# Optimization experiments

Hardware: AMD Instinct MI355X
Metric: run time of the kernel (lower is better)

The kernel has to match this reference:

```python
import jax, jax.numpy as jnp
import numpy as np

N = 50000          # nodes
M_UND = 500000     # undirected edges -> E = 2*M_UND directed messages
Q = 16             # num_groups
MAX_ITER = 10
BP_MAX_DIFF = 0.01


def setup_inputs() -> dict:
    key = jax.random.key(0)
    k1, k2, k3, k4 = jax.random.split(key, 4)
    u = jax.random.randint(k1, (M_UND,), 0, N)
    v = jax.random.randint(k2, (M_UND,), 0, N)
    # each undirected edge (u,v) yields directed messages u->v and v->u
    src = jnp.concatenate([u, v]).astype(jnp.int32)
    dst = jnp.concatenate([v, u]).astype(jnp.int32)
    rev = jnp.concatenate([jnp.arange(M_UND) + M_UND, jnp.arange(M_UND)]).astype(jnp.int32)
    psi0 = jax.random.uniform(k3, (N, Q), dtype=jnp.float32)
    psi0 = psi0 / psi0.sum(1, keepdims=True)
    msg0 = jax.random.uniform(k4, (2 * M_UND, Q), dtype=jnp.float32)
    msg0 = msg0 / msg0.sum(1, keepdims=True)
    c = 2.0 * M_UND / N  # mean degree
    beta = jnp.float32(np.log(Q / np.sqrt(c - 1.0) + 1.0))  # beta_ast init
    return dict(src=src, dst=dst, rev=rev, psi0=psi0, msg0=msg0, beta=beta, n_nodes=N)


def _bp_forward(src, dst, rev, psi0, msg0, beta, n_nodes):
    q = psi0.shape[1]
    n_edges = msg0.shape[0]
    mean_w = float(n_edges) / (float(n_nodes) * float(n_nodes))  # W.mean() for 0/1 weights
    expb_m1 = jnp.exp(beta) - 1.0
    h0 = (-beta * mean_w * psi0).sum(0)  # external field, shape [q]

    def step(carry, _):
        msg, psi, h, done = carry
        # S_e = 1 + psi_{src->dst} * (e^{beta*w} - 1), w == 1
        logS = jnp.log1p(msg * expb_m1)                                    # [E, q]
        node_log = jax.ops.segment_sum(logS, dst, num_segments=n_nodes)    # prod over incoming, log-domain
        # cavity update: message i->j uses all incoming to i except j->i (rev edge)
        new_msg = jax.nn.softmax(node_log[src] - logS[rev] + h, axis=-1)   # exp(h)*prod, normalized
        diff = jnp.max(jnp.abs(jax.lax.stop_gradient(new_msg) -
                               jax.lax.stop_gradient(msg)).sum(-1))
        logS2 = jnp.log1p(new_msg * expb_m1)
        node_log2 = jax.ops.segment_sum(logS2, dst, num_segments=n_nodes)
        new_psi = jax.nn.softmax(node_log2 + h, axis=-1)                    # marginals
        new_h = (-beta * mean_w * new_psi).sum(0)
        # freeze state once converged (mirrors early-return on max_diff < bp_max_diff)
        msg = jnp.where(done, msg, new_msg)
        psi = jnp.where(done, psi, new_psi)
        h = jnp.where(done, h, new_h)
        done = done | (diff < BP_MAX_DIFF)
        return (msg, psi, h, done), diff

    (msg, psi, h, done), _ = jax.lax.scan(
        step, (msg0, psi0, h0, jnp.array(False)), None, length=MAX_ITER)

    # soft modularity: (1/2m) sum_e psi_i . psi_j - sum_g (sum_i d_i psi_ig / 2m)^2
    m2 = float(n_edges)  # total directed edge weight (= 2m for unit weights)
    deg = jax.ops.segment_sum(jnp.ones((n_edges,), psi.dtype), dst, num_segments=n_nodes)
    edge_term = jnp.einsum('eq,eq->', psi[src], psi[dst]) / m2
    deg_term = jnp.sum((jnp.einsum('n,nq->q', deg, psi) / m2) ** 2)
    modularity = edge_term - deg_term
    # group-balance regularizer, scaled by sqrt(q) as in forward()
    reg = jnp.sum((psi.sum(0) / float(n_nodes) - 1.0 / q) ** 2) * np.sqrt(q)
    # mean per-node entropy of marginals, normalized by log(q)
    entropy_loss = jnp.mean(-jnp.sum(psi * jnp.log(psi + 1e-12), axis=-1)) / np.log(q)
    return psi, reg, entropy_loss, modularity


def reference(src, dst, rev, psi0, msg0, beta, n_nodes):
    return _bp_forward(src, dst, rev, psi0, msg0, beta, n_nodes)
```

## Files before the change

kernel.cpp:

```cpp
#include <hip/hip_runtime.h>

#define Q 16
#define SCAN_B 256

__device__ __forceinline__ float wsum(float v){
  #pragma unroll
  for(int o=32;o;o>>=1) v += __shfl_xor(v,o);
  return v;
}
__device__ __forceinline__ float wmaxr(float v){
  #pragma unroll
  for(int o=32;o;o>>=1) v = fmaxf(v,__shfl_xor(v,o));
  return v;
}

__global__ void __launch_bounds__(256, 8) k_edgeF(
    const int* __restrict__ src, const int* __restrict__ dst,
    const int* __restrict__ ipos,
    float* msgC, const float* __restrict__ nl,
    const float* __restrict__ betap,
    const float* __restrict__ hsrc, int nch,
    const float* __restrict__ diffprev, int nbd,
    float* __restrict__ diffout, float* __restrict__ hout,
    int* __restrict__ donep, int M, float mean_w, int k)
{
  if (*donep) return;
  const float beta = *betap;
  const float eb = __expf(beta) - 1.0f;
  const int t = threadIdx.x;
  __shared__ float smf[16][17];
  __shared__ float hq_sm[16];
  __shared__ float smx[4];
  __shared__ int brk;
  {
    const int g = t>>4, qq = t&15;
    float s = 0.0f;
    for (int r = g; r < nch; r += 16) s += hsrc[(size_t)r*Q + qq];
    smf[g][qq] = s; __syncthreads();
    if (t < Q){
      float tot = 0.0f;
      #pragma unroll
      for (int i=0;i<16;i++) tot += smf[i][t];
      hq_sm[t] = -beta * mean_w * tot;
    }
  }
  if (k > 0){
    float dm = 0.0f;
    for (int i = t; i < nbd; i += 256) dm = fmaxf(dm, diffprev[i]);
    dm = wmaxr(dm);
    if ((t & 63) == 0) smx[t>>6] = dm;
    __syncthreads();
    if (t == 0)
      brk = (fmaxf(fmaxf(smx[0],smx[1]), fmaxf(smx[2],smx[3])) < 0.01f);
    __syncthreads();
    if (brk){ if (blockIdx.x == 0 && t == 0) *donep = 1; return; }
  } else {
    __syncthreads();
  }
  if (blockIdx.x == 0 && t < Q) hout[t] = hq_sm[t];
  const float hq = hq_sm[t & 15];

  const int q = t & 15;
  const int grp  = (blockIdx.x*blockDim.x + t) >> 4;
  const int ngrp = (gridDim.x*blockDim.x) >> 4;
  float dloc = 0.0f;
  int p = grp;
  for (; p + ngrp < M; p += 2*ngrp){
    const int pA = p, pB = p + ngrp;
    const int uA = src[pA], vA = dst[pA];
    const int uB = src[pB], vB = dst[pB];
    const int a0 = ipos[pA], a1 = ipos[pA + M];
    const int b0 = ipos[pB], b1 = ipos[pB + M];
    const float mA0 = msgC[(size_t)a0*Q + q], mA1 = msgC[(size_t)a1*Q + q];
    const float mB0 = msgC[(size_t)b0*Q + q], mB1 = msgC[(size_t)b1*Q + q];
    const float nuA = nl[(size_t)uA*Q + q],  nvA = nl[(size_t)vA*Q + q];
    const float nuB = nl[(size_t)uB*Q + q],  nvB = nl[(size_t)vB*Q + q];
    float tA0 = nuA - __logf(fmaf(mA1, eb, 1.0f)) + hq;
    float tA1 = nvA - __logf(fmaf(mA0, eb, 1.0f)) + hq;
    float tB0 = nuB - __logf(fmaf(mB1, eb, 1.0f)) + hq;
    float tB1 = nvB - __logf(fmaf(mB0, eb, 1.0f)) + hq;
    float xA0=tA0, xA1=tA1, xB0=tB0, xB1=tB1;
    #pragma unroll
    for (int o=1;o<16;o<<=1){
      xA0=fmaxf(xA0,__shfl_xor(xA0,o)); xA1=fmaxf(xA1,__shfl_xor(xA1,o));
      xB0=fmaxf(xB0,__shfl_xor(xB0,o)); xB1=fmaxf(xB1,__shfl_xor(xB1,o));
    }
    const float eA0=__expf(tA0-xA0), eA1=__expf(tA1-xA1);
    const float eB0=__expf(tB0-xB0), eB1=__expf(tB1-xB1);
    float sA0=eA0, sA1=eA1, sB0=eB0, sB1=eB1;
    #pragma unroll
    for (int o=1;o<16;o<<=1){
      sA0+=__shfl_xor(sA0,o); sA1+=__shfl_xor(sA1,o);
      sB0+=__shfl_xor(sB0,o); sB1+=__shfl_xor(sB1,o);
    }
    const float nA0=eA0/sA0, nA1=eA1/sA1, nB0=eB0/sB0, nB1=eB1/sB1;
    float dA0=fabsf(nA0-mA0), dA1=fabsf(nA1-mA1);
    float dB0=fabsf(nB0-mB0), dB1=fabsf(nB1-mB1);
    #pragma unroll
    for (int o=1;o<16;o<<=1){
      dA0+=__shfl_xor(dA0,o); dA1+=__shfl_xor(dA1,o);
      dB0+=__shfl_xor(dB0,o); dB1+=__shfl_xor(dB1,o);
    }
    dloc = fmaxf(dloc, fmaxf(fmaxf(dA0,dA1), fmaxf(dB0,dB1)));
    msgC[(size_t)a0*Q + q] = nA0;  msgC[(size_t)a1*Q + q] = nA1;
    msgC[(size_t)b0*Q + q] = nB0;  msgC[(size_t)b1*Q + q] = nB1;
  }
  if (p < M){
    const int u = src[p], v = dst[p];
    const int i0 = ipos[p], i1 = ipos[p + M];
    const float m0 = msgC[(size_t)i0*Q + q], m1 = msgC[(size_t)i1*Q + q];
    const float nu = nl[(size_t)u*Q + q],   nv = nl[(size_t)v*Q + q];
    float t0 = nu - __logf(fmaf(m1, eb, 1.0f)) + hq;
    float t1 = nv - __logf(fmaf(m0, eb, 1.0f)) + hq;
    float x0=t0, x1=t1;
    #pragma unroll
    for (int o=1;o<16;o<<=1){
      x0=fmaxf(x0,__shfl_xor(x0,o)); x1=fmaxf(x1,__shfl_xor(x1,o));
    }
    const float e0=__expf(t0-x0), e1=__expf(t1-x1);
    float s0=e0, s1=e1;
    #pragma unroll
    for (int o=1;o<16;o<<=1){ s0+=__shfl_xor(s0,o); s1+=__shfl_xor(s1,o); }
    const float n0=e0/s0, n1=e1/s1;
    float d0=fabsf(n0-m0), d1=fabsf(n1-m1);
    #pragma unroll
    for (int o=1;o<16;o<<=1){ d0+=__shfl_xor(d0,o); d1+=__shfl_xor(d1,o); }
    dloc = fmaxf(dloc, fmaxf(d0,d1));
    msgC[(size_t)i0*Q + q] = n0;  msgC[(size_t)i1*Q + q] = n1;
  }
  float wm = wmaxr(dloc);
  if ((t & 63) == 0) smx[t>>6] = wm;
  __syncthreads();
  if (t == 0)
    diffout[blockIdx.x] = fmaxf(fmaxf(smx[0],smx[1]), fmaxf(smx[2],smx[3]));
}

__global__ void __launch_bounds__(256, 8) k_gatherF2(
    const float* __restrict__ msgC, const int* __restrict__ offs,
    float* __restrict__ nl, const float* __restrict__ hk,
    float* __restrict__ psi, const float* __restrict__ betap,
    const int* __restrict__ donep, float* __restrict__ hp2k,
    int N, int mode)
{
  if (mode && *donep) return;
  const int wid = threadIdx.x >> 6;
  const int n = blockIdx.x*4 + wid;
  const float eb = __expf(*betap) - 1.0f;
  const int lane = threadIdx.x & 63;
  const int sub = lane >> 4, q16 = lane & 15;
  int start = 0, end = 0;
  if (n < N){ start = offs[n]; end = offs[n+1]; }
  float acc = 0.0f;
  int i = start + sub;
  for (; i + 4 < end; i += 8){
    const float x0 = msgC[(size_t)i*Q + q16];
    const float x1 = msgC[(size_t)(i+4)*Q + q16];
    acc += __logf(fmaf(x0, eb, 1.0f)) + __logf(fmaf(x1, eb, 1.0f));
  }
  if (i < end) acc += __logf(fmaf(msgC[(size_t)i*Q + q16], eb, 1.0f));
  acc += __shfl_xor(acc, 16);
  acc += __shfl_xor(acc, 32);
  if (n < N && sub == 0) nl[(size_t)n*Q + q16] = acc;
  if (!mode) return;
  float t = acc + hk[q16];
  float m = t;
  #pragma unroll
  for (int o=1;o<16;o<<=1) m = fmaxf(m, __shfl_xor(m,o));
  float ex = __expf(t-m);
  float s = ex;
  #pragma unroll
  for (int o=1;o<16;o<<=1) s += __shfl_xor(s,o);
  const float pq = ex/s;
  if (n < N && sub == 0) psi[(size_t)n*Q + q16] = pq;
  __shared__ float smh[4][17];
  if (sub == 0) smh[wid][q16] = (n < N) ? pq : 0.0f;
  __syncthreads();
  if (threadIdx.x < Q)
    unsafeAtomicAdd(&hp2k[(size_t)(blockIdx.x>>6)*Q + threadIdx.x],
      smh[0][threadIdx.x]+smh[1][threadIdx.x]+smh[2][threadIdx.x]+smh[3][threadIdx.x]);
}

__global__ void __launch_bounds__(256, 8) k_h_part(
    const float* __restrict__ psi, float* __restrict__ hpart, int N)
{
  const int n = blockIdx.x*blockDim.x + threadIdx.x;
  float pv[Q];
  if (n < N) {
    const float4* a = (const float4*)(psi + (size_t)n*Q);
    #pragma unroll
    for (int i=0;i<4;i++){ float4 t=a[i]; pv[4*i]=t.x; pv[4*i+1]=t.y; pv[4*i+2]=t.z; pv[4*i+3]=t.w; }
  } else {
    #pragma unroll
    for (int q=0;q<Q;q++) pv[q]=0.0f;
  }
  __shared__ float sm[4][Q];
  const int wid = threadIdx.x>>6, lane = threadIdx.x&63;
  #pragma unroll
  for (int q=0;q<Q;q++){
    float s = wsum(pv[q]);
    if (lane == 0) sm[wid][q] = s;
  }
  __syncthreads();
  if (threadIdx.x < Q)
    hpart[(size_t)blockIdx.x*Q + threadIdx.x] =
      sm[0][threadIdx.x]+sm[1][threadIdx.x]+sm[2][threadIdx.x]+sm[3][threadIdx.x];
}

__global__ void __launch_bounds__(256, 8) k_deg(
    const int* __restrict__ dst, int* __restrict__ deg, int E)
{
  const int e = blockIdx.x*blockDim.x + threadIdx.x;
  if (e < E) atomicAdd(&deg[dst[e]], 1);
}

__global__ void __launch_bounds__(SCAN_B) k_scan1(
    const int* __restrict__ deg, int* __restrict__ offs,
    int* __restrict__ bsum, int N)
{
  __shared__ int sm[SCAN_B];
  const int i = blockIdx.x*SCAN_B + threadIdx.x;
  const int v = (i<N) ? deg[i] : 0;
  sm[threadIdx.x] = v; __syncthreads();
  #pragma unroll
  for (int o=1;o<SCAN_B;o<<=1){
    int t = (threadIdx.x>=o) ? sm[threadIdx.x-o] : 0;
    __syncthreads();
    sm[threadIdx.x] += t;
    __syncthreads();
  }
  if (i<N) offs[i] = sm[threadIdx.x] - v;
  if (threadIdx.x==SCAN_B-1) bsum[blockIdx.x] = sm[threadIdx.x];
}

__global__ void __launch_bounds__(SCAN_B) k_scan2(int* __restrict__ bsum, int nb)
{
  __shared__ int sm[SCAN_B];
  const int v = (threadIdx.x<nb) ? bsum[threadIdx.x] : 0;
  sm[threadIdx.x] = v; __syncthreads();
  #pragma unroll
  for (int o=1;o<SCAN_B;o<<=1){
    int t = (threadIdx.x>=o) ? sm[threadIdx.x-o] : 0;
    __syncthreads();
    sm[threadIdx.x] += t;
    __syncthreads();
  }
  if (threadIdx.x<nb) bsum[threadIdx.x] = sm[threadIdx.x] - v;
}

__global__ void __launch_bounds__(SCAN_B) k_scan3(
    int* __restrict__ offs, int* __restrict__ cursor,
    const int* __restrict__ bsum, int N, int E)
{
  const int i = blockIdx.x*SCAN_B + threadIdx.x;
  if (i<N){
    const int o = offs[i] + bsum[blockIdx.x];
    offs[i] = o; cursor[i] = o;
  }
  if (i==0) offs[N] = E;
}

__global__ void __launch_bounds__(256, 8) k_fillCS(
    const int* __restrict__ dst, int* __restrict__ cursor,
    const float* __restrict__ msg0, float* __restrict__ msgC,
    int* __restrict__ ipos, int E)
{
  const int e = blockIdx.x*blockDim.x + threadIdx.x;
  if (e >= E) return;
  const int ip = atomicAdd(&cursor[dst[e]], 1);
  ipos[e] = ip;
  const float4* s = (const float4*)(msg0 + (size_t)e*Q);
  float4* d = (float4*)(msgC + (size_t)ip*Q);
  float4 x0=s[0], x1=s[1], x2=s[2], x3=s[3];
  d[0]=x0; d[1]=x1; d[2]=x2; d[3]=x3;
}

__global__ void __launch_bounds__(256, 8) k_stats(
    const int* __restrict__ src, const int* __restrict__ dst,
    const float* __restrict__ psi, const int* __restrict__ deg,
    float* __restrict__ colpart, float* __restrict__ degpart,
    float* __restrict__ entpart, float* __restrict__ edgepart,
    int* __restrict__ cnt, float* __restrict__ out,
    int M, int N, int NQ, float m2, int gS)
{
  const int t = threadIdx.x;
  const int lane = t & 63, wid = t >> 6;
  float ed = 0.0f;
  for (int p = blockIdx.x*256 + t; p < M; p += gS*256){
    const int u = src[p], v = dst[p];
    const float4* a = (const float4*)(psi + (size_t)u*Q);
    const float4* b = (const float4*)(psi + (size_t)v*Q);
    float d = 0.0f;
    #pragma unroll
    for (int i=0;i<4;i++){
      float4 x=a[i], y=b[i];
      d += x.x*y.x + x.y*y.y + x.z*y.z + x.w*y.w;
    }
    ed += 2.0f*d;
  }
  float ca[Q], da[Q]; float ea = 0.0f;
  #pragma unroll
  for (int q=0;q<Q;q++){ ca[q]=0.0f; da[q]=0.0f; }
  for (int n = blockIdx.x*256 + t; n < N; n += gS*256){
    const float4* a = (const float4*)(psi + (size_t)n*Q);
    float pv[Q];
    #pragma unroll
    for (int i=0;i<4;i++){ float4 x=a[i]; pv[4*i]=x.x; pv[4*i+1]=x.y; pv[4*i+2]=x.z; pv[4*i+3]=x.w; }
    const float dg = (float)deg[n];
    #pragma unroll
    for (int q=0;q<Q;q++){
      ca[q] += pv[q];
      da[q] += pv[q]*dg;
      ea    -= pv[q]*__logf(pv[q]+1e-12f);
    }
  }
  __shared__ float smc[4][17], smd[4][17];
  __shared__ float sme[4], smeE[4];
  __shared__ float smg[16][17], smg2[16][17];
  __shared__ int amL;
  #pragma unroll
  for (int q=0;q<Q;q++){
    float s  = wsum(ca[q]);
    float s2 = wsum(da[q]);
    if (lane == 0){ smc[wid][q]=s; smd[wid][q]=s2; }
  }
  float se = wsum(ea);
  float sed = wsum(ed);
  if (lane == 0){ sme[wid]=se; smeE[wid]=sed; }
  __syncthreads();
  if (t < Q){
    colpart[(size_t)blockIdx.x*Q+t] = smc[0][t]+smc[1][t]+smc[2][t]+smc[3][t];
    degpart[(size_t)blockIdx.x*Q+t] = smd[0][t]+smd[1][t]+smd[2][t]+smd[3][t];
  }
  if (t == 0){
    entpart[blockIdx.x]  = sme[0]+sme[1]+sme[2]+sme[3];
    edgepart[blockIdx.x] = smeE[0]+smeE[1]+smeE[2]+smeE[3];
  }
  __threadfence();
  if (t == 0) amL = (atomicAdd(cnt, 1) == gS-1);
  __syncthreads();
  if (!amL) return;
  {
    const int g = t>>4, qq = t&15;
    float cs=0.0f, ds=0.0f;
    for (int r = g; r < gS; r += 16){
      cs += colpart[(size_t)r*Q + qq];
      ds += degpart[(size_t)r*Q + qq];
    }
    smg[g][qq] = cs; smg2[g][qq] = ds;
    __syncthreads();
    float colq=0.0f, degq=0.0f;
    if (t < Q){
      #pragma unroll
      for (int i=0;i<16;i++){ colq += smg[i][t]; degq += smg2[i][t]; }
    }
    float es=0.0f, en=0.0f;
    for (int i=t; i<gS; i+=256){ es += edgepart[i]; en += entpart[i]; }
    es = wsum(es); en = wsum(en);
    if (lane == 0){ smeE[wid]=es; sme[wid]=en; }
    __syncthreads();
    if (t < Q){ smg[0][t] = colq; smg2[0][t] = degq; }
    __syncthreads();
    if (t == 0){
      const float edge_total = smeE[0]+smeE[1]+smeE[2]+smeE[3];
      const float ent_total  = sme[0]+sme[1]+sme[2]+sme[3];
      float reg = 0.0f, dt = 0.0f;
      for (int i=0;i<Q;i++){
        float d = smg[0][i]/(float)N - 1.0f/(float)Q; reg += d*d;
        float s = smg2[0][i]/m2; dt += s*s;
      }
      out[NQ+0] = reg * 4.0f;
      out[NQ+1] = ent_total/(float)N / 2.7725887222397811f;
      out[NQ+2] = edge_total/m2 - dt;
    }
  }
}

extern "C" void kernel_launch(void* const* d_in, const int* in_sizes, int n_in,
                              void* d_out, int out_size, void* d_ws, size_t ws_size,
                              hipStream_t stream)
{
  const int*   src   = (const int*)  d_in[0];
  const int*   dst   = (const int*)  d_in[1];
  const float* psi0  = (const float*)d_in[3];
  const float* msg0  = (const float*)d_in[4];
  const float* betap = (const float*)d_in[5];

  const int E  = in_sizes[0];
  const int M  = E/2;
  const int NQ = in_sizes[3];
  const int N  = NQ/Q;
  const float mean_w = (float)((double)E/((double)N*(double)N));
  const float m2 = (float)E;

  const int B = 256;
  const int gE = (E+B-1)/B, gN = (N+B-1)/B;
  const int nb = (N+SCAN_B-1)/SCAN_B;
  const int nbE = 2048;
  const int gW = (N+3)/4;
  const int nchG = (gW+63)>>6;
  const int gS = 256;

  char* w = (char*)d_ws;
  float* msgC    = (float*)w; w += (size_t)E*Q*sizeof(float);
  float* nl      = (float*)w; w += (size_t)NQ*sizeof(float);
  int*   ipos    = (int*)  w; w += (size_t)E*sizeof(int);
  int*   offs    = (int*)  w; w += (size_t)(N+16)*sizeof(int);
  int*   cursor  = (int*)  w; w += (size_t)(N+16)*sizeof(int);
  int*   bsum    = (int*)  w; w += 256*sizeof(int);
  float* hp0     = (float*)w; w += (size_t)gN*Q*sizeof(float);
  float* edgepart= (float*)w; w += (size_t)gS*sizeof(float);
  float* colpart = (float*)w; w += (size_t)gS*Q*sizeof(float);
  float* degpart = (float*)w; w += (size_t)gS*Q*sizeof(float);
  float* entpart = (float*)w; w += (size_t)gS*sizeof(float);
  int*   deg     = (int*)  w; w += (size_t)(N+16)*sizeof(int);
  float* hpart2  = (float*)w; w += (size_t)10*nchG*Q*sizeof(float);
  float* diffpart= (float*)w; w += (size_t)10*nbE*sizeof(float);
  float* harr    = (float*)w; w += (size_t)10*Q*sizeof(float);
  int*   donep   = (int*)  w; w += 4*sizeof(int);
  int*   cnts    = (int*)  w; w += 4*sizeof(int);

  float* psi = (float*)d_out;

  const size_t small_bytes = (size_t)((char*)w - (char*)deg);
  hipMemsetAsync(deg, 0, small_bytes, stream);

  k_h_part  <<<gN,B,0,stream>>>(psi0, hp0, N);
  k_deg     <<<gE,B,0,stream>>>(dst, deg, E);
  k_scan1   <<<nb,SCAN_B,0,stream>>>(deg, offs, bsum, N);
  k_scan2   <<<1, SCAN_B,0,stream>>>(bsum, nb);
  k_scan3   <<<nb,SCAN_B,0,stream>>>(offs, cursor, bsum, N, E);
  k_fillCS  <<<gE,B,0,stream>>>(dst, cursor, msg0, msgC, ipos, E);
  k_gatherF2<<<gW,B,0,stream>>>(msgC, offs, nl, harr, psi, betap, donep,
                                hpart2, N, 0);

  for (int k=0; k<10; ++k) {
    const float* hs  = (k==0) ? hp0 : (hpart2 + (size_t)(k-1)*nchG*Q);
    const int    nch = (k==0) ? gN : nchG;
    const float* dp  = diffpart + (size_t)(k>0 ? k-1 : 0)*nbE;
    k_edgeF   <<<nbE,B,0,stream>>>(src, dst, ipos, msgC, nl, betap,
                                   hs, nch, dp, nbE,
                                   diffpart + (size_t)k*nbE, harr + (size_t)k*Q,
                                   donep, M, mean_w, k);
    k_gatherF2<<<gW,B,0,stream>>>(msgC, offs, nl, harr + (size_t)k*Q, psi,
                                  betap, donep,
                                  hpart2 + (size_t)k*nchG*Q, N, 1);
  }

  k_stats<<<gS,B,0,stream>>>(src, dst, psi, deg, colpart, degpart,
                             entpart, edgepart, cnts, psi, M, N, NQ, m2, gS);
}
```

Measured before the change: 966.1 us.

## Keep edge-ordered message copy for coalesced reads alongside CSR-ordered copy

The edge kernel now reads messages from an edge-ordered buffer (msgA, or msg0 on the first iteration) with contiguous indexing instead of scattered reads through ipos into the CSR-sorted buffer. It writes results to both the edge-ordered buffer and the CSR-ordered buffer (msgB) that the gather kernel consumes. The two-way manual unroll of the edge loop is also removed. This trades random reads for an extra full write of the message array each iteration and doubles workspace size.

```diff
diff --git a/kernel.cpp b/kernel.cpp
--- a/kernel.cpp
+++ b/kernel.cpp
@@ -17,7 +17,8 @@
 __global__ void __launch_bounds__(256, 8) k_edgeF(
     const int* __restrict__ src, const int* __restrict__ dst,
     const int* __restrict__ ipos,
-    float* msgC, const float* __restrict__ nl,
+    const float* __restrict__ msgIn, float* __restrict__ msgA,
+    float* __restrict__ msgB, const float* __restrict__ nl,
     const float* __restrict__ betap,
     const float* __restrict__ hsrc, int nch,
     const float* __restrict__ diffprev, int nbd,
@@ -64,52 +65,13 @@
   const int grp  = (blockIdx.x*blockDim.x + t) >> 4;
   const int ngrp = (gridDim.x*blockDim.x) >> 4;
   float dloc = 0.0f;
-  int p = grp;
-  for (; p + ngrp < M; p += 2*ngrp){
-    const int pA = p, pB = p + ngrp;
-    const int uA = src[pA], vA = dst[pA];
-    const int uB = src[pB], vB = dst[pB];
-    const int a0 = ipos[pA], a1 = ipos[pA + M];
-    const int b0 = ipos[pB], b1 = ipos[pB + M];
-    const float mA0 = msgC[(size_t)a0*Q + q], mA1 = msgC[(size_t)a1*Q + q];
-    const float mB0 = msgC[(size_t)b0*Q + q], mB1 = msgC[(size_t)b1*Q + q];
-    const float nuA = nl[(size_t)uA*Q + q],  nvA = nl[(size_t)vA*Q + q];
-    const float nuB = nl[(size_t)uB*Q + q],  nvB = nl[(size_t)vB*Q + q];
-    float tA0 = nuA - __logf(fmaf(mA1, eb, 1.0f)) + hq;
-    float tA1 = nvA - __logf(fmaf(mA0, eb, 1.0f)) + hq;
-    float tB0 = nuB - __logf(fmaf(mB1, eb, 1.0f)) + hq;
-    float tB1 = nvB - __logf(fmaf(mB0, eb, 1.0f)) + hq;
-    float xA0=tA0, xA1=tA1, xB0=tB0, xB1=tB1;
-    #pragma unroll
-    for (int o=1;o<16;o<<=1){
-      xA0=fmaxf(xA0,__shfl_xor(xA0,o)); xA1=fmaxf(xA1,__shfl_xor(xA1,o));
-      xB0=fmaxf(xB0,__shfl_xor(xB0,o)); xB1=fmaxf(xB1,__shfl_xor(xB1,o));
-    }
-    const float eA0=__expf(tA0-xA0), eA1=__expf(tA1-xA1);
-    const float eB0=__expf(tB0-xB0), eB1=__expf(tB1-xB1);
-    float sA0=eA0, sA1=eA1, sB0=eB0, sB1=eB1;
-    #pragma unroll
-    for (int o=1;o<16;o<<=1){
-      sA0+=__shfl_xor(sA0,o); sA1+=__shfl_xor(sA1,o);
-      sB0+=__shfl_xor(sB0,o); sB1+=__shfl_xor(sB1,o);
-    }
-    const float nA0=eA0/sA0, nA1=eA1/sA1, nB0=eB0/sB0, nB1=eB1/sB1;
-    float dA0=fabsf(nA0-mA0), dA1=fabsf(nA1-mA1);
-    float dB0=fabsf(nB0-mB0), dB1=fabsf(nB1-mB1);
-    #pragma unroll
-    for (int o=1;o<16;o<<=1){
-      dA0+=__shfl_xor(dA0,o); dA1+=__shfl_xor(dA1,o);
-      dB0+=__shfl_xor(dB0,o); dB1+=__shfl_xor(dB1,o);
-    }
-    dloc = fmaxf(dloc, fmaxf(fmaxf(dA0,dA1), fmaxf(dB0,dB1)));
-    msgC[(size_t)a0*Q + q] = nA0;  msgC[(size_t)a1*Q + q] = nA1;
-    msgC[(size_t)b0*Q + q] = nB0;  msgC[(size_t)b1*Q + q] = nB1;
-  }
-  if (p < M){
+  for (int p = grp; p < M; p += ngrp){
     const int u = src[p], v = dst[p];
     const int i0 = ipos[p], i1 = ipos[p + M];
-    const float m0 = msgC[(size_t)i0*Q + q], m1 = msgC[(size_t)i1*Q + q];
-    const float nu = nl[(size_t)u*Q + q],   nv = nl[(size_t)v*Q + q];
+    const float m0 = msgIn[(size_t)p*Q + q];
+    const float m1 = msgIn[((size_t)p + (size_t)M)*Q + q];
+    const float nu = nl[(size_t)u*Q + q];
+    const float nv = nl[(size_t)v*Q + q];
     float t0 = nu - __logf(fmaf(m1, eb, 1.0f)) + hq;
     float t1 = nv - __logf(fmaf(m0, eb, 1.0f)) + hq;
     float x0=t0, x1=t1;
@@ -126,7 +88,10 @@
     #pragma unroll
     for (int o=1;o<16;o<<=1){ d0+=__shfl_xor(d0,o); d1+=__shfl_xor(d1,o); }
     dloc = fmaxf(dloc, fmaxf(d0,d1));
-    msgC[(size_t)i0*Q + q] = n0;  msgC[(size_t)i1*Q + q] = n1;
+    msgA[(size_t)p*Q + q] = n0;
+    msgA[((size_t)p + (size_t)M)*Q + q] = n1;
+    msgB[(size_t)i0*Q + q] = n0;
+    msgB[(size_t)i1*Q + q] = n1;
   }
   float wm = wmaxr(dloc);
   if ((t & 63) == 0) smx[t>>6] = wm;
@@ -136,7 +101,7 @@
 }
 
 __global__ void __launch_bounds__(256, 8) k_gatherF2(
-    const float* __restrict__ msgC, const int* __restrict__ offs,
+    const float* __restrict__ msgB, const int* __restrict__ offs,
     float* __restrict__ nl, const float* __restrict__ hk,
     float* __restrict__ psi, const float* __restrict__ betap,
     const int* __restrict__ donep, float* __restrict__ hp2k,
@@ -153,11 +118,11 @@
   float acc = 0.0f;
   int i = start + sub;
   for (; i + 4 < end; i += 8){
-    const float x0 = msgC[(size_t)i*Q + q16];
-    const float x1 = msgC[(size_t)(i+4)*Q + q16];
+    const float x0 = msgB[(size_t)i*Q + q16];
+    const float x1 = msgB[(size_t)(i+4)*Q + q16];
     acc += __logf(fmaf(x0, eb, 1.0f)) + __logf(fmaf(x1, eb, 1.0f));
   }
-  if (i < end) acc += __logf(fmaf(msgC[(size_t)i*Q + q16], eb, 1.0f));
+  if (i < end) acc += __logf(fmaf(msgB[(size_t)i*Q + q16], eb, 1.0f));
   acc += __shfl_xor(acc, 16);
   acc += __shfl_xor(acc, 32);
   if (n < N && sub == 0) nl[(size_t)n*Q + q16] = acc;
@@ -261,7 +226,7 @@
 
 __global__ void __launch_bounds__(256, 8) k_fillCS(
     const int* __restrict__ dst, int* __restrict__ cursor,
-    const float* __restrict__ msg0, float* __restrict__ msgC,
+    const float* __restrict__ msg0, float* __restrict__ msgB,
     int* __restrict__ ipos, int E)
 {
   const int e = blockIdx.x*blockDim.x + threadIdx.x;
@@ -269,7 +234,7 @@
   const int ip = atomicAdd(&cursor[dst[e]], 1);
   ipos[e] = ip;
   const float4* s = (const float4*)(msg0 + (size_t)e*Q);
-  float4* d = (float4*)(msgC + (size_t)ip*Q);
+  float4* d = (float4*)(msgB + (size_t)ip*Q);
   float4 x0=s[0], x1=s[1], x2=s[2], x3=s[3];
   d[0]=x0; d[1]=x1; d[2]=x2; d[3]=x3;
 }
@@ -401,7 +366,8 @@
   const int gS = 256;
 
   char* w = (char*)d_ws;
-  float* msgC    = (float*)w; w += (size_t)E*Q*sizeof(float);
+  float* msgA    = (float*)w; w += (size_t)E*Q*sizeof(float);
+  float* msgB    = (float*)w; w += (size_t)E*Q*sizeof(float);
   float* nl      = (float*)w; w += (size_t)NQ*sizeof(float);
   int*   ipos    = (int*)  w; w += (size_t)E*sizeof(int);
   int*   offs    = (int*)  w; w += (size_t)(N+16)*sizeof(int);
@@ -429,19 +395,20 @@
   k_scan1   <<<nb,SCAN_B,0,stream>>>(deg, offs, bsum, N);
   k_scan2   <<<1, SCAN_B,0,stream>>>(bsum, nb);
   k_scan3   <<<nb,SCAN_B,0,stream>>>(offs, cursor, bsum, N, E);
-  k_fillCS  <<<gE,B,0,stream>>>(dst, cursor, msg0, msgC, ipos, E);
-  k_gatherF2<<<gW,B,0,stream>>>(msgC, offs, nl, harr, psi, betap, donep,
+  k_fillCS  <<<gE,B,0,stream>>>(dst, cursor, msg0, msgB, ipos, E);
+  k_gatherF2<<<gW,B,0,stream>>>(msgB, offs, nl, harr, psi, betap, donep,
                                 hpart2, N, 0);
 
   for (int k=0; k<10; ++k) {
+    const float* mi  = (k==0) ? msg0 : msgA;
     const float* hs  = (k==0) ? hp0 : (hpart2 + (size_t)(k-1)*nchG*Q);
     const int    nch = (k==0) ? gN : nchG;
     const float* dp  = diffpart + (size_t)(k>0 ? k-1 : 0)*nbE;
-    k_edgeF   <<<nbE,B,0,stream>>>(src, dst, ipos, msgC, nl, betap,
+    k_edgeF   <<<nbE,B,0,stream>>>(src, dst, ipos, mi, msgA, msgB, nl, betap,
                                    hs, nch, dp, nbE,
                                    diffpart + (size_t)k*nbE, harr + (size_t)k*Q,
                                    donep, M, mean_w, k);
-    k_gatherF2<<<gW,B,0,stream>>>(msgC, offs, nl, harr + (size_t)k*Q, psi,
+    k_gatherF2<<<gW,B,0,stream>>>(msgB, offs, nl, harr + (size_t)k*Q, psi,
                                   betap, donep,
                                   hpart2 + (size_t)k*nchG*Q, N, 1);
   }
```

New measurement: 967.9 us. About the same (+0.2%).
